# Performance work log

Hardware: AMD Instinct MI355X
Metric: run time of the kernel (lower is better)

The kernel has to match this reference:

```python
import jax, jax.numpy as jnp
import numpy as np

N_ = 50000   # nodes
E_ = 800000  # edges
G_ = 64      # graphs in batch
EPS = 1e-5   # batchnorm eps


def _lin(k, fi, fo):
    s = 1.0 / np.sqrt(fi)
    return jax.random.uniform(k, (fi, fo), jnp.float32, -s, s)


def setup_inputs() -> dict:
    key = jax.random.key(0)
    ks = jax.random.split(key, 16)
    d_in, d_h, d_out = 128, 128, 5000
    inp = {
        'x': jax.random.normal(ks[0], (N_, d_in), jnp.float32),
        'edge_index': jax.random.randint(ks[1], (2, E_), 0, N_, jnp.int32),
        'batch': jnp.sort(jax.random.randint(ks[2], (N_,), 0, G_, jnp.int32)),
    }
    dims = [(d_in, d_h), (d_h, d_h), (d_h, d_h), (d_h, d_h)]
    for i, (fi, fo) in enumerate(dims, 1):
        inp[f'w{i}'] = _lin(ks[2 + i], fi, fo)
        inp[f'b{i}'] = jnp.zeros((fo,), jnp.float32)
        inp[f'g{i}'] = jnp.ones((fo,), jnp.float32)   # BN gamma
        inp[f'be{i}'] = jnp.zeros((fo,), jnp.float32)  # BN beta
    inp['gw1'] = _lin(ks[7], d_h, d_h // 2)
    inp['gb1'] = jnp.zeros((d_h // 2,), jnp.float32)
    inp['gw2'] = _lin(ks[8], d_h // 2, 1)
    inp['gb2'] = jnp.zeros((1,), jnp.float32)
    inp['cw'] = _lin(ks[9], d_h, d_out)
    inp['cb'] = jnp.zeros((d_out,), jnp.float32)
    return inp


def reference(x, w1, b1, g1, be1, w2, b2, g2, be2, w3, b3, g3, be3,
              w4, b4, g4, be4, gw1, gb1, gw2, gb2, cw, cb,
              edge_index, batch):
    # GCN normalization with self-loops (PyG GCNConv semantics)
    loops = jnp.arange(N_, dtype=edge_index.dtype)
    src = jnp.concatenate([edge_index[0], loops])
    dst = jnp.concatenate([edge_index[1], loops])
    deg = jax.ops.segment_sum(jnp.ones(src.shape[0], jnp.float32), dst, N_)
    dis = jax.lax.rsqrt(jnp.maximum(deg, 1.0))  # deg >= 1 with self-loops
    norm = dis[src] * dis[dst]                  # [E+N]

    def gcn(h, w, b):
        hw = h @ w                              # [N, d]
        msg = hw[src] * norm[:, None]           # gather over edges
        return jax.ops.segment_sum(msg, dst, N_) + b

    def bn(h, g, be):
        m = h.mean(0)
        v = h.var(0)                            # biased var (training BN)
        return (h - m) * jax.lax.rsqrt(v + EPS) * g + be

    h = x
    for w, b, g, be in ((w1, b1, g1, be1), (w2, b2, g2, be2),
                        (w3, b3, g3, be3), (w4, b4, g4, be4)):
        h = jax.nn.relu(bn(gcn(h, w, b), g, be))  # dropout is identity (eval)

    # attention pooling: per-graph softmax over gate scores
    gate = jax.nn.relu(h @ gw1 + gb1) @ gw2 + gb2  # [N, 1]
    gate = gate[:, 0]
    m = jax.ops.segment_max(gate, batch, G_)
    e = jnp.exp(gate - m[batch])
    s = jax.ops.segment_sum(e, batch, G_)
    a = e / s[batch]                               # [N]
    pooled = jax.ops.segment_sum(h * a[:, None], batch, G_)  # [G, d]
    return pooled @ cw + cb                        # [G, out]
```

## Files before the change

### kernel.cpp

```cpp
#include <hip/hip_runtime.h>
#include <hip/hip_bf16.h>
#include <hip/hip_fp16.h>

#define NN   50000
#define NE   800000
#define NG   64
#define DH   128
#define DOUT 5000
#define BNEPS 1e-5f
#define NBLK 196

typedef _Float16 h8 __attribute__((ext_vector_type(8)));
typedef float    f4 __attribute__((ext_vector_type(4)));

__global__ __launch_bounds__(256) void k_count(const int* __restrict__ dst, int* __restrict__ cnt) {
    int e = blockIdx.x * 256 + threadIdx.x;
    if (e < NE) atomicAdd(&cnt[dst[e]], 1);
}

__global__ __launch_bounds__(256) void k_blkscan(const int* __restrict__ cnt, int* __restrict__ rowptr,
                                                 int* __restrict__ bsum) {
    __shared__ int s[256];
    int t = threadIdx.x, i = blockIdx.x * 256 + t;
    int v = (i < NN) ? cnt[i] : 0;
    s[t] = v;
    __syncthreads();
    for (int off = 1; off < 256; off <<= 1) {
        int x = (t >= off) ? s[t - off] : 0;
        __syncthreads();
        s[t] += x;
        __syncthreads();
    }
    if (i < NN) rowptr[i] = s[t] - v;
    if (t == 255) bsum[blockIdx.x] = s[255];
}

__global__ __launch_bounds__(256) void k_bscan(const int* __restrict__ bsum, int* __restrict__ boff) {
    __shared__ int s[256];
    int t = threadIdx.x;
    int v = (t < NBLK) ? bsum[t] : 0;
    s[t] = v;
    __syncthreads();
    for (int off = 1; off < 256; off <<= 1) {
        int x = (t >= off) ? s[t - off] : 0;
        __syncthreads();
        s[t] += x;
        __syncthreads();
    }
    if (t < NBLK) boff[t] = s[t] - v;
}

__global__ __launch_bounds__(256) void k_fin(int* __restrict__ rowptr, const int* __restrict__ boff,
                                             int* __restrict__ cnt, float* __restrict__ dis) {
    int i = blockIdx.x * 256 + threadIdx.x;
    if (i >= NN) { if (i == NN) rowptr[NN] = NE; return; }
    rowptr[i] += boff[blockIdx.x];
    dis[i] = rsqrtf((float)(cnt[i] + 1));
    cnt[i] = 0;
}

__global__ __launch_bounds__(256) void k_fill(const int* __restrict__ ei, const int* __restrict__ rowptr,
                                              int* __restrict__ fil, const float* __restrict__ dis,
                                              int* __restrict__ col, float* __restrict__ wgt) {
    int e = blockIdx.x * 256 + threadIdx.x;
    if (e >= NE) return;
    int s = ei[e], d = ei[NE + e];
    int p = rowptr[d] + atomicAdd(&fil[d], 1);
    col[p] = s;
    wgt[p] = dis[s] * dis[d];
}

__global__ __launch_bounds__(256) void k_wprep(const float* __restrict__ W0, const float* __restrict__ W1,
                                               const float* __restrict__ W2, const float* __restrict__ W3,
                                               __half* __restrict__ Wt) {
    const float* Ws[4] = {W0, W1, W2, W3};
    int m = blockIdx.x >> 4;
    int chunk = blockIdx.x & 15;
    const float* W = Ws[m];
    __half* O = Wt + m * DH * DH;
    int o = chunk * 1024 + threadIdx.x;
    for (int r = 0; r < 4; r++, o += 256) {
        int c = o >> 7, k = o & 127;
        O[o] = __float2half(W[k * DH + c]);
    }
}

__global__ __launch_bounds__(256) void k_gemm3(const float* __restrict__ X, const __half* __restrict__ Wt,
                                               const float* __restrict__ scale, const float* __restrict__ shift,
                                               __half* __restrict__ Y) {
    int t = threadIdx.x;
    int lane = t & 63, wid = t >> 6;
    int wr = wid >> 1, wc = wid & 1;
    int row0 = blockIdx.x * 64;
    int lr = lane & 15, lk = (lane >> 4) * 8;

    f4 acc[2][4];
#pragma unroll
    for (int i = 0; i < 2; i++)
#pragma unroll
        for (int j = 0; j < 4; j++) acc[i][j] = (f4){0.f, 0.f, 0.f, 0.f};

    for (int kt = 0; kt < 4; kt++) {
        int kbase = kt * 32 + lk;
        h8 afr[2];
#pragma unroll
        for (int fr = 0; fr < 2; fr++) {
            int gr = row0 + wr * 32 + fr * 16 + lr;
            gr = min(gr, NN - 1);
            const float4* p = (const float4*)(X + (size_t)gr * DH + kbase);
            float4 v0 = p[0], v1 = p[1];
            if (scale) {
                const float4* sc4 = (const float4*)(scale + kbase);
                const float4* sh4 = (const float4*)(shift + kbase);
                float4 s0 = sc4[0], s1 = sc4[1], h0 = sh4[0], h1 = sh4[1];
                v0.x = fmaxf(fmaf(v0.x, s0.x, h0.x), 0.f);
                v0.y = fmaxf(fmaf(v0.y, s0.y, h0.y), 0.f);
                v0.z = fmaxf(fmaf(v0.z, s0.z, h0.z), 0.f);
                v0.w = fmaxf(fmaf(v0.w, s0.w, h0.w), 0.f);
                v1.x = fmaxf(fmaf(v1.x, s1.x, h1.x), 0.f);
                v1.y = fmaxf(fmaf(v1.y, s1.y, h1.y), 0.f);
                v1.z = fmaxf(fmaf(v1.z, s1.z, h1.z), 0.f);
                v1.w = fmaxf(fmaf(v1.w, s1.w, h1.w), 0.f);
            }
            h8 a;
            a[0] = (_Float16)v0.x; a[1] = (_Float16)v0.y; a[2] = (_Float16)v0.z; a[3] = (_Float16)v0.w;
            a[4] = (_Float16)v1.x; a[5] = (_Float16)v1.y; a[6] = (_Float16)v1.z; a[7] = (_Float16)v1.w;
            afr[fr] = a;
        }
#pragma unroll
        for (int fc = 0; fc < 4; fc++) {
            int gc = wc * 64 + fc * 16 + lr;
            h8 b = *(const h8*)(Wt + (size_t)gc * DH + kbase);
#pragma unroll
            for (int fr = 0; fr < 2; fr++)
                acc[fr][fc] = __builtin_amdgcn_mfma_f32_16x16x32_f16(afr[fr], b, acc[fr][fc], 0, 0, 0);
        }
    }
#pragma unroll
    for (int fr = 0; fr < 2; fr++) {
#pragma unroll
        for (int fc = 0; fc < 4; fc++) {
            int C = wc * 64 + fc * 16 + lr;
#pragma unroll
            for (int q = 0; q < 4; q++) {
                int R = row0 + wr * 32 + fr * 16 + (lane >> 4) * 4 + q;
                if (R < NN) Y[(size_t)R * DH + C] = __float2half(acc[fr][fc][q]);
            }
        }
    }
}

__global__ __launch_bounds__(256) void k_agg(const __half* __restrict__ HW, const int* __restrict__ rowptr,
                                             const int* __restrict__ col, const float* __restrict__ wgt,
                                             const float* __restrict__ dis, const float* __restrict__ bias,
                                             float* __restrict__ OUT, float* __restrict__ ssum,
                                             float* __restrict__ ssq) {
    __shared__ float lsum[DH], lsq[DH];
    int t = threadIdx.x;
    if (t < DH) { lsum[t] = 0.f; lsq[t] = 0.f; }
    __syncthreads();
    int wid = t >> 6, lane = t & 63;
    int sub = lane >> 5, sl = lane & 31;
    const int2* HW4 = (const int2*)HW;
    float4* OUT4 = (float4*)OUT;
    float4 bv = ((const float4*)bias)[sl];
    float s0 = 0, s1 = 0, s2 = 0, s3 = 0, q0 = 0, q1 = 0, q2 = 0, q3 = 0;
    int gw = blockIdx.x * 4 + wid;
    for (int i = gw * 2 + sub; i < NN; i += 16384) {
        float sd = dis[i];
        int2 hr = HW4[i * 32 + sl];
        float2 f0 = __half22float2(*(__half2*)&hr.x);
        float2 f1 = __half22float2(*(__half2*)&hr.y);
        float a0 = sd * sd * f0.x, a1 = sd * sd * f0.y;
        float a2 = sd * sd * f1.x, a3 = sd * sd * f1.y;
        int p = rowptr[i], p1 = rowptr[i + 1];
        for (; p + 4 <= p1; p += 4) {
            int c0 = col[p], c1 = col[p + 1], c2 = col[p + 2], c3 = col[p + 3];
            float w0 = wgt[p], w1 = wgt[p + 1], w2 = wgt[p + 2], w3 = wgt[p + 3];
            int2 r0 = HW4[c0 * 32 + sl];
            int2 r1 = HW4[c1 * 32 + sl];
            int2 r2 = HW4[c2 * 32 + sl];
            int2 r3 = HW4[c3 * 32 + sl];
            float2 g0 = __half22float2(*(__half2*)&r0.x), g1 = __half22float2(*(__half2*)&r0.y);
            a0 = fmaf(w0, g0.x, a0); a1 = fmaf(w0, g0.y, a1); a2 = fmaf(w0, g1.x, a2); a3 = fmaf(w0, g1.y, a3);
            g0 = __half22float2(*(__half2*)&r1.x); g1 = __half22float2(*(__half2*)&r1.y);
            a0 = fmaf(w1, g0.x, a0); a1 = fmaf(w1, g0.y, a1); a2 = fmaf(w1, g1.x, a2); a3 = fmaf(w1, g1.y, a3);
            g0 = __half22float2(*(__half2*)&r2.x); g1 = __half22float2(*(__half2*)&r2.y);
            a0 = fmaf(w2, g0.x, a0); a1 = fmaf(w2, g0.y, a1); a2 = fmaf(w2, g1.x, a2); a3 = fmaf(w2, g1.y, a3);
            g0 = __half22float2(*(__half2*)&r3.x); g1 = __half22float2(*(__half2*)&r3.y);
            a0 = fmaf(w3, g0.x, a0); a1 = fmaf(w3, g0.y, a1); a2 = fmaf(w3, g1.x, a2); a3 = fmaf(w3, g1.y, a3);
        }
        for (; p < p1; p++) {
            int c = col[p];
            float wv = wgt[p];
            int2 r = HW4[c * 32 + sl];
            float2 g0 = __half22float2(*(__half2*)&r.x), g1 = __half22float2(*(__half2*)&r.y);
            a0 = fmaf(wv, g0.x, a0); a1 = fmaf(wv, g0.y, a1);
            a2 = fmaf(wv, g1.x, a2); a3 = fmaf(wv, g1.y, a3);
        }
        a0 += bv.x; a1 += bv.y; a2 += bv.z; a3 += bv.w;
        OUT4[i * 32 + sl] = make_float4(a0, a1, a2, a3);
        s0 += a0; s1 += a1; s2 += a2; s3 += a3;
        q0 += a0 * a0; q1 += a1 * a1; q2 += a2 * a2; q3 += a3 * a3;
    }
    atomicAdd(&lsum[sl * 4 + 0], s0); atomicAdd(&lsum[sl * 4 + 1], s1);
    atomicAdd(&lsum[sl * 4 + 2], s2); atomicAdd(&lsum[sl * 4 + 3], s3);
    atomicAdd(&lsq[sl * 4 + 0], q0);  atomicAdd(&lsq[sl * 4 + 1], q1);
    atomicAdd(&lsq[sl * 4 + 2], q2);  atomicAdd(&lsq[sl * 4 + 3], q3);
    __syncthreads();
    if (t < DH) { atomicAdd(&ssum[t], lsum[t]); atomicAdd(&ssq[t], lsq[t]); }
}

__global__ void k_bnfin(float* __restrict__ ssum, float* __restrict__ ssq,
                        const float* __restrict__ g, const float* __restrict__ be,
                        float* __restrict__ scale, float* __restrict__ shift) {
    int f = threadIdx.x;
    float m = ssum[f] * (1.f / NN);
    float v = ssq[f] * (1.f / NN) - m * m;
    float r = rsqrtf(v + BNEPS);
    float sc = r * g[f];
    scale[f] = sc;
    shift[f] = fmaf(-m, sc, be[f]);
    ssum[f] = 0.f;
    ssq[f] = 0.f;
}

__global__ __launch_bounds__(256) void k_gate(const float* __restrict__ H, const float* __restrict__ scale,
                                              const float* __restrict__ shift, const float* __restrict__ gw1,
                                              const float* __restrict__ gb1, const float* __restrict__ gw2,
                                              const float* __restrict__ gb2, float* __restrict__ gate) {
    __shared__ float w1s[DH * 64];
    __shared__ float rowbuf[4][DH];
    int t = threadIdx.x;
    for (int i = t; i < DH * 64; i += 256) w1s[i] = gw1[i];
    __syncthreads();
    int wid = t >> 6, lane = t & 63;
    float b1v = gb1[lane], w2v = gw2[lane], b2v = gb2[0];
    float2 sc2 = ((const float2*)scale)[lane];
    float2 sh2 = ((const float2*)shift)[lane];
    int nw = gridDim.x * 4;
    int iters = (NN + nw - 1) / nw;
    const float2* H2 = (const float2*)H;
    for (int it = 0; it < iters; it++) {
        int i = blockIdx.x * 4 + wid + it * nw;
        bool act = i < NN;
        if (act) {
            float2 hv = H2[i * 64 + lane];
            rowbuf[wid][lane * 2] = fmaxf(fmaf(hv.x, sc2.x, sh2.x), 0.f);
            rowbuf[wid][lane * 2 + 1] = fmaxf(fmaf(hv.y, sc2.y, sh2.y), 0.f);
        }
        __syncthreads();
        float hid = 0.f;
#pragma unroll 8
        for (int k = 0; k < DH; k++) hid = fmaf(rowbuf[wid][k], w1s[k * 64 + lane], hid);
        hid = fmaxf(hid + b1v, 0.f);
        float v = hid * w2v;
        for (int off = 32; off > 0; off >>= 1) v += __shfl_down(v, off, 64);
        if (act && lane == 0) gate[i] = v + b2v;
        __syncthreads();
    }
}

__device__ __forceinline__ int lbound(const int* __restrict__ a, int v) {
    int lo = 0, hi = NN;
    while (lo < hi) {
        int mid = (lo + hi) >> 1;
        if (a[mid] < v) lo = mid + 1; else hi = mid;
    }
    return lo;
}

__global__ __launch_bounds__(256) void k_pms(const float* __restrict__ gate, const int* __restrict__ batch,
                                             float* __restrict__ ms, float* __restrict__ pooled) {
    __shared__ float red[256];
    int g = blockIdx.x, t = threadIdx.x;
    if (t < DH) pooled[g * DH + t] = 0.f;
    int s = lbound(batch, g), e = lbound(batch, g + 1);
    float m = -INFINITY;
    for (int i = s + t; i < e; i += 256) m = fmaxf(m, gate[i]);
    red[t] = m; __syncthreads();
    for (int off = 128; off > 0; off >>= 1) { if (t < off) red[t] = fmaxf(red[t], red[t + off]); __syncthreads(); }
    m = red[0];
    __syncthreads();
    float se = 0.f;
    for (int i = s + t; i < e; i += 256) se += __expf(gate[i] - m);
    red[t] = se; __syncthreads();
    for (int off = 128; off > 0; off >>= 1) { if (t < off) red[t] += red[t + off]; __syncthreads(); }
    if (t == 0) {
        ms[g * 2] = m;
        ms[g * 2 + 1] = (e > s) ? 1.f / red[0] : 0.f;
    }
}

#define PNODES 8
__global__ __launch_bounds__(256) void k_pool2(const float* __restrict__ H, const float* __restrict__ scale,
                                               const float* __restrict__ shift, const float* __restrict__ gate,
                                               const int* __restrict__ batch, const float* __restrict__ ms,
                                               float* __restrict__ pooled) {
    int wid = threadIdx.x >> 6, lane = threadIdx.x & 63;
    int base = (blockIdx.x * 4 + wid) * PNODES;
    if (base >= NN) return;
    int end = min(base + PNODES, NN);
    const float2* H2 = (const float2*)H;
    float2 sc2 = ((const float2*)scale)[lane];
    float2 sh2 = ((const float2*)shift)[lane];
    float2 acc = make_float2(0.f, 0.f);
    int curg = batch[base];
    for (int i = base; i < end; i++) {
        int g = batch[i];
        if (g != curg) {
            atomicAdd(&pooled[curg * DH + lane * 2], acc.x);
            atomicAdd(&pooled[curg * DH + lane * 2 + 1], acc.y);
            acc = make_float2(0.f, 0.f);
            curg = g;
        }
        float a = __expf(gate[i] - ms[g * 2]) * ms[g * 2 + 1];
        float2 h = H2[i * 64 + lane];
        float hx = fmaxf(fmaf(h.x, sc2.x, sh2.x), 0.f);
        float hy = fmaxf(fmaf(h.y, sc2.y, sh2.y), 0.f);
        acc.x = fmaf(a, hx, acc.x);
        acc.y = fmaf(a, hy, acc.y);
    }
    atomicAdd(&pooled[curg * DH + lane * 2], acc.x);
    atomicAdd(&pooled[curg * DH + lane * 2 + 1], acc.y);
}

__global__ __launch_bounds__(256) void k_cls(const float* __restrict__ pooled, const float* __restrict__ cw,
                                             const float* __restrict__ cb, float* __restrict__ out) {
    __shared__ float pr[DH];
    int g = blockIdx.y;
    if (threadIdx.x < DH) pr[threadIdx.x] = pooled[g * DH + threadIdx.x];
    __syncthreads();
    int j = blockIdx.x * 256 + threadIdx.x;
    if (j >= DOUT) return;
    float acc = cb[j];
#pragma unroll 8
    for (int k = 0; k < DH; k++) acc = fmaf(pr[k], cw[k * DOUT + j], acc);
    out[g * DOUT + j] = acc;
}

extern "C" void kernel_launch(void* const* d_in, const int* in_sizes, int n_in,
                              void* d_out, int out_size, void* d_ws, size_t ws_size,
                              hipStream_t stream) {
    const float* x     = (const float*)d_in[0];
    const int*   ei    = (const int*)d_in[1];
    const int*   batch = (const int*)d_in[2];
    const float* w[4]  = {(const float*)d_in[3], (const float*)d_in[7], (const float*)d_in[11], (const float*)d_in[15]};
    const float* bb[4] = {(const float*)d_in[4], (const float*)d_in[8], (const float*)d_in[12], (const float*)d_in[16]};
    const float* gg[4] = {(const float*)d_in[5], (const float*)d_in[9], (const float*)d_in[13], (const float*)d_in[17]};
    const float* be[4] = {(const float*)d_in[6], (const float*)d_in[10], (const float*)d_in[14], (const float*)d_in[18]};
    const float* gw1 = (const float*)d_in[19];
    const float* gb1 = (const float*)d_in[20];
    const float* gw2 = (const float*)d_in[21];
    const float* gb2 = (const float*)d_in[22];
    const float* cw  = (const float*)d_in[23];
    const float* cb  = (const float*)d_in[24];

    char* base = (char*)d_ws;
    size_t off = 0;
    auto take = [&](size_t n) -> char* { char* r = base + off; off = (off + n + 255) & ~(size_t)255; return r; };
    float*  bufA   = (float*)take((size_t)NN * DH * 4);
    __half* bufB   = (__half*)take((size_t)NN * DH * 2);
    int*   colv   = (int*)take((size_t)NE * 4);
    float* wgt    = (float*)take((size_t)NE * 4);
    int*   rowptr = (int*)take((size_t)(NN + 1) * 4);
    int*   cnt    = (int*)take((size_t)NN * 4);
    float* dis    = (float*)take((size_t)NN * 4);
    float* gate   = (float*)take((size_t)NN * 4);
    float* stats  = (float*)take(2 * DH * 4);
    float* ssum = stats, *ssq = stats + DH;
    float* scale  = (float*)take(DH * 4);
    float* shift  = (float*)take(DH * 4);
    float* pooled = (float*)take((size_t)NG * DH * 4);
    int*   bsum   = (int*)take((size_t)256 * 4);
    int*   boff   = (int*)take((size_t)256 * 4);
    float* ms     = (float*)take((size_t)NG * 2 * 4);
    __half* Wt    = (__half*)take((size_t)4 * DH * DH * 2);

    hipMemsetAsync(cnt, 0, NN * 4, stream);
    hipMemsetAsync(stats, 0, 2 * DH * 4, stream);
    k_count<<<(NE + 255) / 256, 256, 0, stream>>>(ei + NE, cnt);
    k_blkscan<<<NBLK, 256, 0, stream>>>(cnt, rowptr, bsum);
    k_bscan<<<1, 256, 0, stream>>>(bsum, boff);
    k_fin<<<NBLK, 256, 0, stream>>>(rowptr, boff, cnt, dis);
    k_fill<<<(NE + 255) / 256, 256, 0, stream>>>(ei, rowptr, cnt, dis, colv, wgt);
    k_wprep<<<64, 256, 0, stream>>>(w[0], w[1], w[2], w[3], Wt);

    const int gemm_grid = (NN + 63) / 64;
    for (int L = 0; L < 4; L++) {
        k_gemm3<<<gemm_grid, 256, 0, stream>>>(L == 0 ? x : bufA, Wt + (size_t)L * DH * DH,
                                               L == 0 ? nullptr : scale,
                                               L == 0 ? nullptr : shift, bufB);
        k_agg<<<2048, 256, 0, stream>>>(bufB, rowptr, colv, wgt, dis, bb[L], bufA, ssum, ssq);
        k_bnfin<<<1, DH, 0, stream>>>(ssum, ssq, gg[L], be[L], scale, shift);
    }
    k_gate<<<1024, 256, 0, stream>>>(bufA, scale, shift, gw1, gb1, gw2, gb2, gate);
    k_pms<<<NG, 256, 0, stream>>>(gate, batch, ms, pooled);
    k_pool2<<<(NN + 4 * PNODES - 1) / (4 * PNODES), 256, 0, stream>>>(bufA, scale, shift, gate, batch, ms, pooled);
    k_cls<<<dim3((DOUT + 255) / 256, NG), 256, 0, stream>>>(pooled, cw, cb, (float*)d_out);
}
```

Baseline: 604.9 us.

## Store GEMM output in 16-column slabs and aggregate per slab with edge-parallel lanes

The GEMM now writes its fp16 output as eight column slabs of 16 features (each slab contiguous across nodes). The aggregation kernel assigns each block one slab: a wave processes one node, with 16 lane groups each taking a different edge and 4 lanes covering the slab's 16 columns, then reduces across lane groups with shuffles. The aim is a gather working set per slab small enough to stay in L2/cache and more edges in flight per node. The cost is shuffle reductions, idle lanes for low-degree nodes (average degree ~16), and row indices and weights being read once per slab.

```diff
diff --git a/kernel.cpp b/kernel.cpp
--- a/kernel.cpp
+++ b/kernel.cpp
@@ -140,75 +140,78 @@
     for (int fr = 0; fr < 2; fr++) {
 #pragma unroll
         for (int fc = 0; fc < 4; fc++) {
-            int C = wc * 64 + fc * 16 + lr;
+            __half* Yb = Y + (size_t)(wc * 4 + fc) * NN * 16;
 #pragma unroll
             for (int q = 0; q < 4; q++) {
                 int R = row0 + wr * 32 + fr * 16 + (lane >> 4) * 4 + q;
-                if (R < NN) Y[(size_t)R * DH + C] = __float2half(acc[fr][fc][q]);
+                if (R < NN) Yb[(size_t)R * 16 + lr] = __float2half(acc[fr][fc][q]);
             }
         }
     }
 }
 
-__global__ __launch_bounds__(256) void k_agg(const __half* __restrict__ HW, const int* __restrict__ rowptr,
-                                             const int* __restrict__ col, const float* __restrict__ wgt,
-                                             const float* __restrict__ dis, const float* __restrict__ bias,
-                                             float* __restrict__ OUT, float* __restrict__ ssum,
-                                             float* __restrict__ ssq) {
-    __shared__ float lsum[DH], lsq[DH];
+__global__ __launch_bounds__(256) void k_agg4(const __half* __restrict__ HWs, const int* __restrict__ rowptr,
+                                              const int* __restrict__ col, const float* __restrict__ wgt,
+                                              const float* __restrict__ dis, const float* __restrict__ bias,
+                                              float* __restrict__ OUT, float* __restrict__ ssum,
+                                              float* __restrict__ ssq) {
+    __shared__ float lsum[16], lsq[16];
     int t = threadIdx.x;
-    if (t < DH) { lsum[t] = 0.f; lsq[t] = 0.f; }
-    __syncthreads();
+    if (t < 16) { lsum[t] = 0.f; lsq[t] = 0.f; }
+    __syncthreads();
+    int s = blockIdx.x & 7;
+    int sb = blockIdx.x >> 3;
+    int nsb = gridDim.x >> 3;
     int wid = t >> 6, lane = t & 63;
-    int sub = lane >> 5, sl = lane & 31;
-    const int2* HW4 = (const int2*)HW;
-    float4* OUT4 = (float4*)OUT;
-    float4 bv = ((const float4*)bias)[sl];
+    int q = lane & 3, g = lane >> 2;
+    const int2* HS = (const int2*)HWs + (size_t)s * NN * 4;
+    float4 bv = ((const float4*)bias)[s * 4 + q];
     float s0 = 0, s1 = 0, s2 = 0, s3 = 0, q0 = 0, q1 = 0, q2 = 0, q3 = 0;
-    int gw = blockIdx.x * 4 + wid;
-    for (int i = gw * 2 + sub; i < NN; i += 16384) {
+    int nwave = nsb * 4;
+    for (int i = sb * 4 + wid; i < NN; i += nwave) {
+        int p0 = rowptr[i], p1 = rowptr[i + 1];
         float sd = dis[i];
-        int2 hr = HW4[i * 32 + sl];
-        float2 f0 = __half22float2(*(__half2*)&hr.x);
-        float2 f1 = __half22float2(*(__half2*)&hr.y);
-        float a0 = sd * sd * f0.x, a1 = sd * sd * f0.y;
-        float a2 = sd * sd * f1.x, a3 = sd * sd * f1.y;
-        int p = rowptr[i], p1 = rowptr[i + 1];
-        for (; p + 4 <= p1; p += 4) {
-            int c0 = col[p], c1 = col[p + 1], c2 = col[p + 2], c3 = col[p + 3];
-            float w0 = wgt[p], w1 = wgt[p + 1], w2 = wgt[p + 2], w3 = wgt[p + 3];
-            int2 r0 = HW4[c0 * 32 + sl];
-            int2 r1 = HW4[c1 * 32 + sl];
-            int2 r2 = HW4[c2 * 32 + sl];
-            int2 r3 = HW4[c3 * 32 + sl];
-            float2 g0 = __half22float2(*(__half2*)&r0.x), g1 = __half22float2(*(__half2*)&r0.y);
-            a0 = fmaf(w0, g0.x, a0); a1 = fmaf(w0, g0.y, a1); a2 = fmaf(w0, g1.x, a2); a3 = fmaf(w0, g1.y, a3);
-            g0 = __half22float2(*(__half2*)&r1.x); g1 = __half22float2(*(__half2*)&r1.y);
-            a0 = fmaf(w1, g0.x, a0); a1 = fmaf(w1, g0.y, a1); a2 = fmaf(w1, g1.x, a2); a3 = fmaf(w1, g1.y, a3);
-            g0 = __half22float2(*(__half2*)&r2.x); g1 = __half22float2(*(__half2*)&r2.y);
-            a0 = fmaf(w2, g0.x, a0); a1 = fmaf(w2, g0.y, a1); a2 = fmaf(w2, g1.x, a2); a3 = fmaf(w2, g1.y, a3);
-            g0 = __half22float2(*(__half2*)&r3.x); g1 = __half22float2(*(__half2*)&r3.y);
-            a0 = fmaf(w3, g0.x, a0); a1 = fmaf(w3, g0.y, a1); a2 = fmaf(w3, g1.x, a2); a3 = fmaf(w3, g1.y, a3);
-        }
-        for (; p < p1; p++) {
-            int c = col[p];
-            float wv = wgt[p];
-            int2 r = HW4[c * 32 + sl];
-            float2 g0 = __half22float2(*(__half2*)&r.x), g1 = __half22float2(*(__half2*)&r.y);
-            a0 = fmaf(wv, g0.x, a0); a1 = fmaf(wv, g0.y, a1);
-            a2 = fmaf(wv, g1.x, a2); a3 = fmaf(wv, g1.y, a3);
-        }
-        a0 += bv.x; a1 += bv.y; a2 += bv.z; a3 += bv.w;
-        OUT4[i * 32 + sl] = make_float4(a0, a1, a2, a3);
-        s0 += a0; s1 += a1; s2 += a2; s3 += a3;
-        q0 += a0 * a0; q1 += a1 * a1; q2 += a2 * a2; q3 += a3 * a3;
-    }
-    atomicAdd(&lsum[sl * 4 + 0], s0); atomicAdd(&lsum[sl * 4 + 1], s1);
-    atomicAdd(&lsum[sl * 4 + 2], s2); atomicAdd(&lsum[sl * 4 + 3], s3);
-    atomicAdd(&lsq[sl * 4 + 0], q0);  atomicAdd(&lsq[sl * 4 + 1], q1);
-    atomicAdd(&lsq[sl * 4 + 2], q2);  atomicAdd(&lsq[sl * 4 + 3], q3);
-    __syncthreads();
-    if (t < DH) { atomicAdd(&ssum[t], lsum[t]); atomicAdd(&ssq[t], lsq[t]); }
+        float a0 = 0.f, a1 = 0.f, a2 = 0.f, a3 = 0.f;
+        if (g == 0) {
+            int2 hs = HS[(size_t)i * 4 + q];
+            float2 f0 = __half22float2(*(__half2*)&hs.x);
+            float2 f1 = __half22float2(*(__half2*)&hs.y);
+            float w = sd * sd;
+            a0 = w * f0.x; a1 = w * f0.y; a2 = w * f1.x; a3 = w * f1.y;
+        }
+        for (int p = p0; p < p1; p += 16) {
+            int idx = p + g;
+            bool v = idx < p1;
+            int c = v ? col[idx] : 0;
+            float w = v ? wgt[idx] : 0.f;
+            int2 r = HS[(size_t)c * 4 + q];
+            float2 f0 = __half22float2(*(__half2*)&r.x);
+            float2 f1 = __half22float2(*(__half2*)&r.y);
+            a0 = fmaf(w, f0.x, a0); a1 = fmaf(w, f0.y, a1);
+            a2 = fmaf(w, f1.x, a2); a3 = fmaf(w, f1.y, a3);
+        }
+#pragma unroll
+        for (int m = 4; m < 64; m <<= 1) {
+            a0 += __shfl_xor(a0, m, 64);
+            a1 += __shfl_xor(a1, m, 64);
+            a2 += __shfl_xor(a2, m, 64);
+            a3 += __shfl_xor(a3, m, 64);
+        }
+        if (g == 0) {
+            a0 += bv.x; a1 += bv.y; a2 += bv.z; a3 += bv.w;
+            ((float4*)(OUT + (size_t)i * DH + s * 16))[q] = make_float4(a0, a1, a2, a3);
+            s0 += a0; s1 += a1; s2 += a2; s3 += a3;
+            q0 += a0 * a0; q1 += a1 * a1; q2 += a2 * a2; q3 += a3 * a3;
+        }
+    }
+    if (g == 0 && wid >= 0) {
+        atomicAdd(&lsum[q * 4 + 0], s0); atomicAdd(&lsum[q * 4 + 1], s1);
+        atomicAdd(&lsum[q * 4 + 2], s2); atomicAdd(&lsum[q * 4 + 3], s3);
+        atomicAdd(&lsq[q * 4 + 0], q0);  atomicAdd(&lsq[q * 4 + 1], q1);
+        atomicAdd(&lsq[q * 4 + 2], q2);  atomicAdd(&lsq[q * 4 + 3], q3);
+    }
+    __syncthreads();
+    if (t < 16) { atomicAdd(&ssum[s * 16 + t], lsum[t]); atomicAdd(&ssq[s * 16 + t], lsq[t]); }
 }
 
 __global__ void k_bnfin(float* __restrict__ ssum, float* __restrict__ ssq,
@@ -391,7 +394,7 @@
         k_gemm3<<<gemm_grid, 256, 0, stream>>>(L == 0 ? x : bufA, Wt + (size_t)L * DH * DH,
                                                L == 0 ? nullptr : scale,
                                                L == 0 ? nullptr : shift, bufB);
-        k_agg<<<2048, 256, 0, stream>>>(bufB, rowptr, colv, wgt, dis, bb[L], bufA, ssum, ssq);
+        k_agg4<<<2048, 256, 0, stream>>>(bufB, rowptr, colv, wgt, dis, bb[L], bufA, ssum, ssq);
         k_bnfin<<<1, DH, 0, stream>>>(ssum, ssq, gg[L], be[L], scale, shift);
     }
     k_gate<<<1024, 256, 0, stream>>>(bufA, scale, shift, gw1, gb1, gw2, gb2, gate);
```

New measurement: 635.5 us. 5.1% more time.
